# Kernel optimization log

Hardware: AMD Instinct MI355X
Metric: run time of the kernel (lower is better)

Reference implementation:

```python
import jax, jax.numpy as jnp
import numpy as np

NUM_CHUNKS = 8
HEAD_DIM = 128
PROJ = 1024       # projection_size (q)
KV_PROJ = 1024    # kv_projection_size
NEG_INF = -1e30


def _rotate_half(x):
    x1, x2 = jnp.split(x, 2, axis=-1)
    return jnp.concatenate((-x2, x1), axis=-1)


def _apply_rope(x, cos, sin):
    # x: [B, S, H, D]; cos/sin: [B, S, 1, rot_dim] with rot_dim == D here
    return x * cos + _rotate_half(x) * sin


def setup_inputs() -> dict:
    key = jax.random.key(0)
    k1, k2, k3 = jax.random.split(key, 3)
    S, B, H = 8192, 1, 1024
    layernorm_output = jax.random.normal(k1, (S, B, H), dtype=jnp.float32)
    # rotary tables, stored [S, 1, 1, rot_dim] (seq-first, like the torch module)
    inv_freq = 1.0 / (10000.0 ** (jnp.arange(0, HEAD_DIM, 2, dtype=jnp.float32) / HEAD_DIM))
    t = jnp.arange(S, dtype=jnp.float32)
    freqs = jnp.einsum('s,d->sd', t, inv_freq)
    emb = jnp.concatenate((freqs, freqs), axis=-1)  # [S, rot_dim]
    freqs_cos = jnp.cos(emb)[:, None, None, :]
    freqs_sin = jnp.sin(emb)[:, None, None, :]
    qkv_weight = jax.random.normal(k2, (PROJ + 2 * KV_PROJ, H), dtype=jnp.float32) * (H ** -0.5)
    qkv_bias = jax.random.normal(k3, (PROJ + 2 * KV_PROJ,), dtype=jnp.float32) * 0.02
    return {
        'layernorm_output': layernorm_output,
        'freqs_cos': freqs_cos,
        'freqs_sin': freqs_sin,
        'qkv_weight': qkv_weight,
        'qkv_bias': qkv_bias,
    }


def reference(layernorm_output, freqs_cos, freqs_sin, qkv_weight, qkv_bias):
    S, B, H = layernorm_output.shape
    cs = S // NUM_CHUNKS  # chunk size
    scale = HEAD_DIM ** -0.5
    # permute(1,0,2,3): [S,1,1,rot] -> [1,S,1,rot] matching [B, seq, head, dim]
    cos = jnp.transpose(freqs_cos, (1, 0, 2, 3))
    sin = jnp.transpose(freqs_sin, (1, 0, 2, 3))

    outs = []
    k_list, v_list = [], []
    for i in range(NUM_CHUNKS):
        st, ed = i * cs, (i + 1) * cs
        x = layernorm_output[st:ed]                      # [cs, B, H]
        qkv = jnp.einsum('sbh,oh->sbo', x, qkv_weight) + qkv_bias
        def to_bshd(t):
            return jnp.transpose(t.reshape(cs, B, -1, HEAD_DIM), (1, 0, 2, 3))
        q = to_bshd(qkv[..., :PROJ])                     # [B, cs, nH, D]
        k = to_bshd(qkv[..., PROJ:PROJ + KV_PROJ])
        v = to_bshd(qkv[..., PROJ + KV_PROJ:])
        cos_i, sin_i = cos[:, st:ed], sin[:, st:ed]
        q = _apply_rope(q, cos_i, sin_i)
        k = _apply_rope(k, cos_i, sin_i)
        k_list.append(k)
        v_list.append(v)

        K = jnp.concatenate(k_list, axis=1)              # [B, (i+1)*cs, nH, D]
        V = jnp.concatenate(v_list, axis=1)
        scores = jnp.einsum('bqhd,bkhd->bhqk', q, K) * scale
        # causal: query global idx st+r attends keys <= st+r; earlier chunks fully visible
        qidx = st + jnp.arange(cs)
        kidx = jnp.arange((i + 1) * cs)
        mask = kidx[None, :] <= qidx[:, None]            # [cs, (i+1)*cs]
        scores = jnp.where(mask[None, None], scores, NEG_INF)
        p = jax.nn.softmax(scores, axis=-1)
        outs.append(jnp.einsum('bhqk,bkhd->bqhd', p, V))
    return jnp.concatenate(outs, axis=1)                 # [B, S, nH, D]
```

## Files before the change

### kernel.cpp

```cpp
#include <hip/hip_runtime.h>
#include <hip/hip_bf16.h>

typedef float f32x4 __attribute__((ext_vector_type(4)));
typedef __bf16 bf16x8 __attribute__((ext_vector_type(8)));
typedef __bf16 bf16x4 __attribute__((ext_vector_type(4)));

#define S_LEN 8192
#define HIDDEN 1024
#define NH 8
#define HD 128

#define QSCALE (0.08838834764831845f * 1.4426950408889634f)
#define FIXMAX 24.0f

__device__ __forceinline__ void async16(const void* g, void* l) {
  __builtin_amdgcn_global_load_lds(
      (const __attribute__((address_space(1))) char*)g,
      (__attribute__((address_space(3))) char*)l, 16, 0, 0);
}

__global__ void cast_bf16_kernel(const float* __restrict__ in, __bf16* __restrict__ out) {
  int i = (blockIdx.x * blockDim.x + threadIdx.x) * 4;
  float4 v = *(const float4*)(in + i);
  bf16x4 o;
  o[0] = (__bf16)v.x; o[1] = (__bf16)v.y; o[2] = (__bf16)v.z; o[3] = (__bf16)v.w;
  *(bf16x4*)(out + i) = o;
}

__global__ __launch_bounds__(256) void gemm_qkv(
    const __bf16* __restrict__ A, const __bf16* __restrict__ W,
    const float* __restrict__ bias,
    __bf16* __restrict__ Qb, __bf16* __restrict__ Kb, __bf16* __restrict__ Vt)
{
  __shared__ __bf16 As[128 * 32];
  __shared__ __bf16 Bs[128 * 32];
  const int t = threadIdx.x;
  const int lane = t & 63;
  const int w = t >> 6;
  const int wy = w >> 1, wx = w & 1;
  const int quad = lane >> 4, l15 = lane & 15;
  const int m0 = blockIdx.y * 128;
  const int n0 = blockIdx.x * 128;
  f32x4 acc[4][4] = {};
  for (int kt = 0; kt < HIDDEN; kt += 32) {
#pragma unroll
    for (int j = 0; j < 2; ++j) {
      int idx = j * 256 + t;
      int row = idx >> 2, c8 = (idx & 3) * 8;
      async16(A + (size_t)(m0 + row) * HIDDEN + kt + c8, As + idx * 8);
      async16(W + (size_t)(n0 + row) * HIDDEN + kt + c8, Bs + idx * 8);
    }
    __syncthreads();
    bf16x8 af[4], bfr[4];
#pragma unroll
    for (int i = 0; i < 4; ++i)
      af[i] = *(const bf16x8*)(As + (wy * 64 + i * 16 + l15) * 32 + quad * 8);
#pragma unroll
    for (int i = 0; i < 4; ++i)
      bfr[i] = *(const bf16x8*)(Bs + (wx * 64 + i * 16 + l15) * 32 + quad * 8);
#pragma unroll
    for (int mt = 0; mt < 4; ++mt)
#pragma unroll
      for (int nt = 0; nt < 4; ++nt)
        acc[mt][nt] = __builtin_amdgcn_mfma_f32_16x16x32_bf16(af[mt], bfr[nt], acc[mt][nt], 0, 0, 0);
    __syncthreads();
  }
  float bv[4];
  int cols[4];
#pragma unroll
  for (int nt = 0; nt < 4; ++nt) {
    cols[nt] = n0 + wx * 64 + nt * 16 + l15;
    bv[nt] = bias[cols[nt]];
  }
#pragma unroll
  for (int mt = 0; mt < 4; ++mt) {
    int srow_base = m0 + wy * 64 + mt * 16 + quad * 4;
#pragma unroll
    for (int nt = 0; nt < 4; ++nt) {
      int c = cols[nt];
#pragma unroll
      for (int r = 0; r < 4; ++r) {
        int s = srow_base + r;
        __bf16 b = (__bf16)(acc[mt][nt][r] + bv[nt]);
        if (n0 < 1024) {
          int h = c >> 7, d = c & 127;
          Qb[(size_t)h * S_LEN * HD + (size_t)s * HD + d] = b;
        } else if (n0 < 2048) {
          int c2 = c - 1024; int h = c2 >> 7, d = c2 & 127;
          Kb[(size_t)h * S_LEN * HD + (size_t)s * HD + d] = b;
        } else {
          int c2 = c - 2048; int h = c2 >> 7, d = c2 & 127;
          Vt[(size_t)h * HD * S_LEN + (size_t)d * S_LEN + s] = b;
        }
      }
    }
  }
}

__global__ void rope_kernel(__bf16* __restrict__ Qb, __bf16* __restrict__ Kb,
                            const float* __restrict__ fcos, const float* __restrict__ fsin)
{
  int gid = blockIdx.x * blockDim.x + threadIdx.x;
  int d = gid & 63;
  int h = (gid >> 6) & 7;
  int s = gid >> 9;
  float c1 = fcos[s * 128 + d],      s1 = fsin[s * 128 + d];
  float c2 = fcos[s * 128 + d + 64], s2 = fsin[s * 128 + d + 64];
  size_t base = (size_t)h * S_LEN * HD + (size_t)s * HD + d;
  float q1 = (float)Qb[base], q2 = (float)Qb[base + 64];
  Qb[base]      = (__bf16)((q1 * c1 - q2 * s1) * QSCALE);
  Qb[base + 64] = (__bf16)((q2 * c2 + q1 * s2) * QSCALE);
  float k1 = (float)Kb[base], k2 = (float)Kb[base + 64];
  Kb[base]      = (__bf16)(k1 * c1 - k2 * s1);
  Kb[base + 64] = (__bf16)(k2 * c2 + k1 * s2);
}

__global__ __launch_bounds__(256, 2) void attn_kernel(
    const __bf16* __restrict__ Qb, const __bf16* __restrict__ Kb,
    const __bf16* __restrict__ Vt, float* __restrict__ out,
    __bf16* __restrict__ partO, float* __restrict__ partML)
{
  __shared__ __bf16 Ks[2][64 * 128];
  __shared__ __bf16 Vs[2][128 * 64];
  __shared__ __bf16 Ps[4 * 16 * 64];
  const int t = threadIdx.x;
  const int lane = t & 63, w = t >> 6;
  const int quad = lane >> 4, l15 = lane & 15;
  const int sw = l15 & 7;
  const int sw4 = (l15 & 3) << 2;

  const int id = blockIdx.x;
  const int k = id / 24, r = id % 24;
  int head, qi, piece, j0, j1;
  bool isPartial;
  if (r < 16) { qi = 63 - k; piece = r >> 3; head = r & 7;
                j0 = piece * (qi + 1); j1 = j0 + (qi + 1); isPartial = true; }
  else        { qi = 31 - k; piece = 0; head = r - 16;
                j0 = 0; j1 = 2 * qi + 2; isPartial = false; }
  const int qs = qi * 128;
  const int jmax_w = 2 * qi + (w >> 1);
  const __bf16* Qh = Qb + (size_t)head * S_LEN * HD;
  const __bf16* Kh = Kb + (size_t)head * S_LEN * HD;
  const __bf16* Vh = Vt + (size_t)head * HD * S_LEN;

  bf16x8 qf[2][4];
#pragma unroll
  for (int qg = 0; qg < 2; ++qg) {
    int qrow = qs + w * 32 + qg * 16 + l15;
#pragma unroll
    for (int dk = 0; dk < 4; ++dk)
      qf[qg][dk] = *(const bf16x8*)(Qh + (size_t)qrow * HD + dk * 32 + quad * 8);
  }

  f32x4 o[2][8] = {};
  float l_loc[2] = {0.f, 0.f};
  const f32x4 FM = {-FIXMAX, -FIXMAX, -FIXMAX, -FIXMAX};

  auto stageK = [&](int j, int sel) {
    const __bf16* Kp = Kh + (size_t)(j * 64) * HD;
    __bf16* Kd = &Ks[sel][0];
#pragma unroll
    for (int li = 0; li < 4; ++li) {
      int slot = li * 256 + t;
      int kr = slot >> 4, cp = slot & 15;
      async16(Kp + (size_t)kr * HD + (cp ^ (kr & 7)) * 8, Kd + slot * 8);
    }
  };
  auto stageV = [&](int j, int sel) {
    const __bf16* Vp = Vh + j * 64;
    __bf16* Vd = &Vs[sel][0];
#pragma unroll
    for (int li = 0; li < 4; ++li) {
      int slot = li * 256 + t;
      int d = slot >> 3, cp = slot & 7;
      async16(Vp + (size_t)d * S_LEN + (cp ^ (d & 7)) * 8, Vd + slot * 8);
    }
  };

  stageK(j0, 0);
  stageV(j0, 0);

  for (int j = j0; j < j1; ++j) {
    __syncthreads();
    const int cur = (j - j0) & 1;
    if (j + 1 < j1) {
      stageK(j + 1, cur ^ 1);
      stageV(j + 1, cur ^ 1);
    }
    if (j > jmax_w) continue;
    const __bf16* Ksb = &Ks[cur][0];
    const __bf16* Vsb = &Vs[cur][0];

    f32x4 sc[2][4];
#pragma unroll
    for (int mtk = 0; mtk < 4; ++mtk) {
      bf16x8 kf = *(const bf16x8*)(Ksb + (mtk * 16 + l15) * 128 + ((quad ^ sw) * 8));
      sc[0][mtk] = __builtin_amdgcn_mfma_f32_16x16x32_bf16(kf, qf[0][0], FM, 0, 0, 0);
      sc[1][mtk] = __builtin_amdgcn_mfma_f32_16x16x32_bf16(kf, qf[1][0], FM, 0, 0, 0);
    }
#pragma unroll
    for (int dk = 1; dk < 4; ++dk)
#pragma unroll
      for (int mtk = 0; mtk < 4; ++mtk) {
        bf16x8 kf = *(const bf16x8*)(Ksb + (mtk * 16 + l15) * 128 + (((dk * 4 + quad) ^ sw) * 8));
        sc[0][mtk] = __builtin_amdgcn_mfma_f32_16x16x32_bf16(kf, qf[0][dk], sc[0][mtk], 0, 0, 0);
        sc[1][mtk] = __builtin_amdgcn_mfma_f32_16x16x32_bf16(kf, qf[1][dk], sc[1][mtk], 0, 0, 0);
      }

    if (j >= 2 * qi && (w >> 1) == (j - 2 * qi)) {
      int wq = (w & 1) * 32;
#pragma unroll
      for (int qg = 0; qg < 2; ++qg)
#pragma unroll
        for (int mtk = 0; mtk < 4; ++mtk)
#pragma unroll
          for (int r2 = 0; r2 < 4; ++r2)
            if (mtk * 16 + quad * 4 + r2 - wq > qg * 16 + l15)
              sc[qg][mtk][r2] = -1e30f;
    }

    bf16x8 vf[2][8];
#pragma unroll
    for (int kb = 0; kb < 2; ++kb)
#pragma unroll
      for (int dt = 0; dt < 8; ++dt)
        vf[kb][dt] = *(const bf16x8*)(Vsb + (dt * 16 + l15) * 64 + (((kb * 4 + quad) ^ sw) * 8));

#pragma unroll
    for (int qg = 0; qg < 2; ++qg) {
#pragma unroll
      for (int mtk = 0; mtk < 4; ++mtk) {
        bf16x4 pk;
#pragma unroll
        for (int r2 = 0; r2 < 4; ++r2) {
          float p = __builtin_amdgcn_exp2f(sc[qg][mtk][r2]);
          l_loc[qg] += p;
          pk[r2] = (__bf16)p;
        }
        int slot = (mtk * 4 + quad) ^ sw4;
        *(bf16x4*)(Ps + w * 1024 + l15 * 64 + slot * 4) = pk;
      }
#pragma unroll
      for (int kb = 0; kb < 2; ++kb) {
        bf16x8 pf = *(const bf16x8*)(Ps + w * 1024 + l15 * 64 + (((kb * 8 + quad * 2) ^ sw4) * 4));
#pragma unroll
        for (int dt = 0; dt < 8; ++dt)
          o[qg][dt] = __builtin_amdgcn_mfma_f32_16x16x32_bf16(vf[kb][dt], pf, o[qg][dt], 0, 0, 0);
      }
    }
  }

  float inv[2], lfull[2];
#pragma unroll
  for (int qg = 0; qg < 2; ++qg) {
    float lv = l_loc[qg];
    lv += __shfl_xor(lv, 16);
    lv += __shfl_xor(lv, 32);
    lfull[qg] = lv;
    inv[qg] = 1.0f / lv;
  }
  if (!isPartial) {
#pragma unroll
    for (int qg = 0; qg < 2; ++qg) {
      int s = qs + w * 32 + qg * 16 + l15;
#pragma unroll
      for (int dt = 0; dt < 8; ++dt) {
        f32x4 v;
#pragma unroll
        for (int r2 = 0; r2 < 4; ++r2) v[r2] = o[qg][dt][r2] * inv[qg];
        *(f32x4*)(out + (size_t)s * 1024 + head * 128 + dt * 16 + quad * 4) = v;
      }
    }
  } else {
    int u = (qi - 32) * 16 + piece * 8 + head;
    __bf16* Op = partO + (size_t)u * 128 * 128;
    float* mlp = partML + u * 256;
#pragma unroll
    for (int qg = 0; qg < 2; ++qg) {
      int row = w * 32 + qg * 16 + l15;
#pragma unroll
      for (int dt = 0; dt < 8; ++dt) {
        bf16x4 pk;
#pragma unroll
        for (int r2 = 0; r2 < 4; ++r2) pk[r2] = (__bf16)(o[qg][dt][r2] * inv[qg]);
        *(bf16x4*)(Op + row * 128 + dt * 16 + quad * 4) = pk;
      }
    }
    if (quad == 0) {
#pragma unroll
      for (int qg = 0; qg < 2; ++qg)
        mlp[w * 32 + qg * 16 + l15] = lfull[qg];
    }
  }
}

__global__ __launch_bounds__(256) void merge_kernel(
    const __bf16* __restrict__ partO, const float* __restrict__ partML,
    float* __restrict__ out)
{
  int b = blockIdx.x;
  int qi = 32 + (b >> 3), head = b & 7;
  int u0 = (qi - 32) * 16 + head;
  int u1 = u0 + 8;
  int t = threadIdx.x;
  int q = t >> 1, dh = (t & 1) * 64;
  float l0 = partML[u0 * 256 + q];
  float l1 = partML[u1 * 256 + q];
  float inv = 1.0f / (l0 + l1);
  float w0 = l0 * inv, w1 = l1 * inv;
  const __bf16* O0 = partO + ((size_t)u0 * 128 + q) * 128 + dh;
  const __bf16* O1 = partO + ((size_t)u1 * 128 + q) * 128 + dh;
  float* op = out + (size_t)(qi * 128 + q) * 1024 + head * 128 + dh;
#pragma unroll
  for (int d = 0; d < 64; d += 8) {
    bf16x8 a = *(const bf16x8*)(O0 + d);
    bf16x8 c = *(const bf16x8*)(O1 + d);
    float4 r0, r1;
    r0.x = w0 * (float)a[0] + w1 * (float)c[0];
    r0.y = w0 * (float)a[1] + w1 * (float)c[1];
    r0.z = w0 * (float)a[2] + w1 * (float)c[2];
    r0.w = w0 * (float)a[3] + w1 * (float)c[3];
    r1.x = w0 * (float)a[4] + w1 * (float)c[4];
    r1.y = w0 * (float)a[5] + w1 * (float)c[5];
    r1.z = w0 * (float)a[6] + w1 * (float)c[6];
    r1.w = w0 * (float)a[7] + w1 * (float)c[7];
    *(float4*)(op + d) = r0;
    *(float4*)(op + d + 4) = r1;
  }
}

extern "C" void kernel_launch(void* const* d_in, const int* in_sizes, int n_in,
                              void* d_out, int out_size, void* d_ws, size_t ws_size,
                              hipStream_t stream)
{
  const float* x    = (const float*)d_in[0];
  const float* fcos = (const float*)d_in[1];
  const float* fsin = (const float*)d_in[2];
  const float* wq   = (const float*)d_in[3];
  const float* bias = (const float*)d_in[4];
  float* out = (float*)d_out;

  char* ws = (char*)d_ws;
  __bf16* xb = (__bf16*)ws;
  __bf16* wb = (__bf16*)(ws + 16777216);
  __bf16* Qb = (__bf16*)(ws + 23068672);
  __bf16* Kb = (__bf16*)(ws + 39845888);
  __bf16* Vt = (__bf16*)(ws + 56623104);

  __bf16* partO = xb;
  float* partML = (float*)wb;

  cast_bf16_kernel<<<8192, 256, 0, stream>>>(x, xb);
  cast_bf16_kernel<<<3072, 256, 0, stream>>>(wq, wb);
  dim3 gg(24, 64);
  gemm_qkv<<<gg, 256, 0, stream>>>(xb, wb, bias, Qb, Kb, Vt);
  rope_kernel<<<16384, 256, 0, stream>>>(Qb, Kb, fcos, fsin);
  attn_kernel<<<768, 256, 0, stream>>>(Qb, Kb, Vt, out, partO, partML);
  merge_kernel<<<256, 256, 0, stream>>>(partO, partML, out);
}
```

Measured before the change: 427.9 us.

## Use 256-row query tiles with 512-thread blocks and split every tile's KV range

Result: slower. 916.8 us (+114.2%).

```diff
diff --git a/kernel.cpp b/kernel.cpp
--- a/kernel.cpp
+++ b/kernel.cpp
@@ -115,14 +115,14 @@
   Kb[base + 64] = (__bf16)(k2 * c2 + k1 * s2);
 }
 
-__global__ __launch_bounds__(256, 2) void attn_kernel(
+__global__ __launch_bounds__(512, 4) void attn_kernel(
     const __bf16* __restrict__ Qb, const __bf16* __restrict__ Kb,
     const __bf16* __restrict__ Vt, float* __restrict__ out,
     __bf16* __restrict__ partO, float* __restrict__ partML)
 {
   __shared__ __bf16 Ks[2][64 * 128];
   __shared__ __bf16 Vs[2][128 * 64];
-  __shared__ __bf16 Ps[4 * 16 * 64];
+  __shared__ __bf16 Ps[8 * 16 * 64];
   const int t = threadIdx.x;
   const int lane = t & 63, w = t >> 6;
   const int quad = lane >> 4, l15 = lane & 15;
@@ -130,15 +130,15 @@
   const int sw4 = (l15 & 3) << 2;
 
   const int id = blockIdx.x;
-  const int k = id / 24, r = id % 24;
-  int head, qi, piece, j0, j1;
-  bool isPartial;
-  if (r < 16) { qi = 63 - k; piece = r >> 3; head = r & 7;
-                j0 = piece * (qi + 1); j1 = j0 + (qi + 1); isPartial = true; }
-  else        { qi = 31 - k; piece = 0; head = r - 16;
-                j0 = 0; j1 = 2 * qi + 2; isPartial = false; }
-  const int qs = qi * 128;
-  const int jmax_w = 2 * qi + (w >> 1);
+  int qs, r;
+  if (id < 256) { qs = 31 - (id >> 4); r = id & 15; }
+  else          { qs = (id - 256) >> 4; r = id & 15; }
+  const int piece = r >> 3, head = r & 7;
+  const int nt = 2 * qs + 2;
+  const int j0 = piece * nt, j1 = j0 + nt;
+  const int jmax_w = 4 * qs + (w >> 1);
+  const int qbase = qs * 256;
+
   const __bf16* Qh = Qb + (size_t)head * S_LEN * HD;
   const __bf16* Kh = Kb + (size_t)head * S_LEN * HD;
   const __bf16* Vh = Vt + (size_t)head * HD * S_LEN;
@@ -146,7 +146,7 @@
   bf16x8 qf[2][4];
 #pragma unroll
   for (int qg = 0; qg < 2; ++qg) {
-    int qrow = qs + w * 32 + qg * 16 + l15;
+    int qrow = qbase + w * 32 + qg * 16 + l15;
 #pragma unroll
     for (int dk = 0; dk < 4; ++dk)
       qf[qg][dk] = *(const bf16x8*)(Qh + (size_t)qrow * HD + dk * 32 + quad * 8);
@@ -160,8 +160,8 @@
     const __bf16* Kp = Kh + (size_t)(j * 64) * HD;
     __bf16* Kd = &Ks[sel][0];
 #pragma unroll
-    for (int li = 0; li < 4; ++li) {
-      int slot = li * 256 + t;
+    for (int li = 0; li < 2; ++li) {
+      int slot = li * 512 + t;
       int kr = slot >> 4, cp = slot & 15;
       async16(Kp + (size_t)kr * HD + (cp ^ (kr & 7)) * 8, Kd + slot * 8);
     }
@@ -170,8 +170,8 @@
     const __bf16* Vp = Vh + j * 64;
     __bf16* Vd = &Vs[sel][0];
 #pragma unroll
-    for (int li = 0; li < 4; ++li) {
-      int slot = li * 256 + t;
+    for (int li = 0; li < 2; ++li) {
+      int slot = li * 512 + t;
       int d = slot >> 3, cp = slot & 7;
       async16(Vp + (size_t)d * S_LEN + (cp ^ (d & 7)) * 8, Vd + slot * 8);
     }
@@ -207,7 +207,7 @@
         sc[1][mtk] = __builtin_amdgcn_mfma_f32_16x16x32_bf16(kf, qf[1][dk], sc[1][mtk], 0, 0, 0);
       }
 
-    if (j >= 2 * qi && (w >> 1) == (j - 2 * qi)) {
+    if (j == jmax_w) {
       int wq = (w & 1) * 32;
 #pragma unroll
       for (int qg = 0; qg < 2; ++qg)
@@ -257,12 +257,12 @@
     lv += __shfl_xor(lv, 16);
     lv += __shfl_xor(lv, 32);
     lfull[qg] = lv;
-    inv[qg] = 1.0f / lv;
-  }
-  if (!isPartial) {
+    inv[qg] = lv > 0.f ? 1.0f / lv : 0.f;
+  }
+  if (piece == 1) {
 #pragma unroll
     for (int qg = 0; qg < 2; ++qg) {
-      int s = qs + w * 32 + qg * 16 + l15;
+      int s = qbase + w * 32 + qg * 16 + l15;
 #pragma unroll
       for (int dt = 0; dt < 8; ++dt) {
         f32x4 v;
@@ -272,9 +272,7 @@
       }
     }
   } else {
-    int u = (qi - 32) * 16 + piece * 8 + head;
-    __bf16* Op = partO + (size_t)u * 128 * 128;
-    float* mlp = partML + u * 256;
+    __bf16* Op = partO + (size_t)(qs * 8 + head) * 256 * 128;
 #pragma unroll
     for (int qg = 0; qg < 2; ++qg) {
       int row = w * 32 + qg * 16 + l15;
@@ -286,6 +284,9 @@
         *(bf16x4*)(Op + row * 128 + dt * 16 + quad * 4) = pk;
       }
     }
+  }
+  {
+    float* mlp = partML + (size_t)(qs * 16 + piece * 8 + head) * 256;
     if (quad == 0) {
 #pragma unroll
       for (int qg = 0; qg < 2; ++qg)
@@ -299,33 +300,26 @@
     float* __restrict__ out)
 {
   int b = blockIdx.x;
-  int qi = 32 + (b >> 3), head = b & 7;
-  int u0 = (qi - 32) * 16 + head;
-  int u1 = u0 + 8;
+  int qs = b >> 3, head = b & 7;
   int t = threadIdx.x;
-  int q = t >> 1, dh = (t & 1) * 64;
-  float l0 = partML[u0 * 256 + q];
-  float l1 = partML[u1 * 256 + q];
-  float inv = 1.0f / (l0 + l1);
-  float w0 = l0 * inv, w1 = l1 * inv;
-  const __bf16* O0 = partO + ((size_t)u0 * 128 + q) * 128 + dh;
-  const __bf16* O1 = partO + ((size_t)u1 * 128 + q) * 128 + dh;
-  float* op = out + (size_t)(qi * 128 + q) * 1024 + head * 128 + dh;
-#pragma unroll
-  for (int d = 0; d < 64; d += 8) {
-    bf16x8 a = *(const bf16x8*)(O0 + d);
-    bf16x8 c = *(const bf16x8*)(O1 + d);
-    float4 r0, r1;
-    r0.x = w0 * (float)a[0] + w1 * (float)c[0];
-    r0.y = w0 * (float)a[1] + w1 * (float)c[1];
-    r0.z = w0 * (float)a[2] + w1 * (float)c[2];
-    r0.w = w0 * (float)a[3] + w1 * (float)c[3];
-    r1.x = w0 * (float)a[4] + w1 * (float)c[4];
-    r1.y = w0 * (float)a[5] + w1 * (float)c[5];
-    r1.z = w0 * (float)a[6] + w1 * (float)c[6];
-    r1.w = w0 * (float)a[7] + w1 * (float)c[7];
-    *(float4*)(op + d) = r0;
-    *(float4*)(op + d + 4) = r1;
+  int dq = (t & 31) * 4;
+  const float* ml0 = partML + (size_t)(qs * 16 + head) * 256;
+  const float* ml1 = partML + (size_t)(qs * 16 + 8 + head) * 256;
+  const __bf16* O0 = partO + (size_t)(qs * 8 + head) * 256 * 128;
+#pragma unroll 4
+  for (int row = t >> 5; row < 256; row += 8) {
+    float l0 = ml0[row];
+    float l1 = ml1[row];
+    float inv = 1.0f / (l0 + l1);
+    float w0 = l0 * inv, w1 = l1 * inv;
+    bf16x4 a = *(const bf16x4*)(O0 + row * 128 + dq);
+    float* op = out + (size_t)(qs * 256 + row) * 1024 + head * 128 + dq;
+    float4 c = *(const float4*)op;
+    c.x = w0 * (float)a[0] + w1 * c.x;
+    c.y = w0 * (float)a[1] + w1 * c.y;
+    c.z = w0 * (float)a[2] + w1 * c.z;
+    c.w = w0 * (float)a[3] + w1 * c.w;
+    *(float4*)op = c;
   }
 }
 
@@ -355,6 +349,6 @@
   dim3 gg(24, 64);
   gemm_qkv<<<gg, 256, 0, stream>>>(xb, wb, bias, Qb, Kb, Vt);
   rope_kernel<<<16384, 256, 0, stream>>>(Qb, Kb, fcos, fsin);
-  attn_kernel<<<768, 256, 0, stream>>>(Qb, Kb, Vt, out, partO, partML);
+  attn_kernel<<<512, 512, 0, stream>>>(Qb, Kb, Vt, out, partO, partML);
   merge_kernel<<<256, 256, 0, stream>>>(partO, partML, out);
 }
```

## Halve attention KV tile to 32 keys and raise occupancy to three blocks

Applied to the files above, without the earlier changes.

Result: faster. 384.2 us (-10.2%).

```diff
diff --git a/kernel.cpp b/kernel.cpp
--- a/kernel.cpp
+++ b/kernel.cpp
@@ -115,30 +115,30 @@
   Kb[base + 64] = (__bf16)(k2 * c2 + k1 * s2);
 }
 
-__global__ __launch_bounds__(256, 2) void attn_kernel(
+__global__ __launch_bounds__(256, 3) void attn_kernel(
     const __bf16* __restrict__ Qb, const __bf16* __restrict__ Kb,
     const __bf16* __restrict__ Vt, float* __restrict__ out,
     __bf16* __restrict__ partO, float* __restrict__ partML)
 {
-  __shared__ __bf16 Ks[2][64 * 128];
-  __shared__ __bf16 Vs[2][128 * 64];
-  __shared__ __bf16 Ps[4 * 16 * 64];
+  __shared__ __bf16 Ks[2][32 * 128];
+  __shared__ __bf16 Vs[2][64 * 64];
+  __shared__ __bf16 Ps[4 * 1024];
   const int t = threadIdx.x;
   const int lane = t & 63, w = t >> 6;
   const int quad = lane >> 4, l15 = lane & 15;
   const int sw = l15 & 7;
-  const int sw4 = (l15 & 3) << 2;
+  const int sw6 = l15 & 6;
 
   const int id = blockIdx.x;
   const int k = id / 24, r = id % 24;
   int head, qi, piece, j0, j1;
   bool isPartial;
   if (r < 16) { qi = 63 - k; piece = r >> 3; head = r & 7;
-                j0 = piece * (qi + 1); j1 = j0 + (qi + 1); isPartial = true; }
+                j0 = piece * (2 * qi + 2); j1 = j0 + (2 * qi + 2); isPartial = true; }
   else        { qi = 31 - k; piece = 0; head = r - 16;
-                j0 = 0; j1 = 2 * qi + 2; isPartial = false; }
+                j0 = 0; j1 = 4 * qi + 4; isPartial = false; }
   const int qs = qi * 128;
-  const int jmax_w = 2 * qi + (w >> 1);
+  const int jmax_w = 4 * qi + w;
   const __bf16* Qh = Qb + (size_t)head * S_LEN * HD;
   const __bf16* Kh = Kb + (size_t)head * S_LEN * HD;
   const __bf16* Vh = Vt + (size_t)head * HD * S_LEN;
@@ -157,23 +157,25 @@
   const f32x4 FM = {-FIXMAX, -FIXMAX, -FIXMAX, -FIXMAX};
 
   auto stageK = [&](int j, int sel) {
-    const __bf16* Kp = Kh + (size_t)(j * 64) * HD;
+    const __bf16* Kp = Kh + (size_t)(j * 32) * HD;
     __bf16* Kd = &Ks[sel][0];
 #pragma unroll
-    for (int li = 0; li < 4; ++li) {
+    for (int li = 0; li < 2; ++li) {
       int slot = li * 256 + t;
       int kr = slot >> 4, cp = slot & 15;
       async16(Kp + (size_t)kr * HD + (cp ^ (kr & 7)) * 8, Kd + slot * 8);
     }
   };
   auto stageV = [&](int j, int sel) {
-    const __bf16* Vp = Vh + j * 64;
+    const __bf16* Vp = Vh + j * 32;
     __bf16* Vd = &Vs[sel][0];
 #pragma unroll
-    for (int li = 0; li < 4; ++li) {
-      int slot = li * 256 + t;
-      int d = slot >> 3, cp = slot & 7;
-      async16(Vp + (size_t)d * S_LEN + (cp ^ (d & 7)) * 8, Vd + slot * 8);
+    for (int li = 0; li < 2; ++li) {
+      int c = li * 256 + t;
+      int rr = c >> 3, sl = c & 7;
+      int slu = sl ^ (rr & 7);
+      int d = 2 * rr + (slu >> 2);
+      async16(Vp + (size_t)d * S_LEN + (slu & 3) * 8, Vd + c * 8);
     }
   };
 
@@ -191,9 +193,9 @@
     const __bf16* Ksb = &Ks[cur][0];
     const __bf16* Vsb = &Vs[cur][0];
 
-    f32x4 sc[2][4];
-#pragma unroll
-    for (int mtk = 0; mtk < 4; ++mtk) {
+    f32x4 sc[2][2];
+#pragma unroll
+    for (int mtk = 0; mtk < 2; ++mtk) {
       bf16x8 kf = *(const bf16x8*)(Ksb + (mtk * 16 + l15) * 128 + ((quad ^ sw) * 8));
       sc[0][mtk] = __builtin_amdgcn_mfma_f32_16x16x32_bf16(kf, qf[0][0], FM, 0, 0, 0);
       sc[1][mtk] = __builtin_amdgcn_mfma_f32_16x16x32_bf16(kf, qf[1][0], FM, 0, 0, 0);
@@ -201,35 +203,27 @@
 #pragma unroll
     for (int dk = 1; dk < 4; ++dk)
 #pragma unroll
-      for (int mtk = 0; mtk < 4; ++mtk) {
+      for (int mtk = 0; mtk < 2; ++mtk) {
         bf16x8 kf = *(const bf16x8*)(Ksb + (mtk * 16 + l15) * 128 + (((dk * 4 + quad) ^ sw) * 8));
         sc[0][mtk] = __builtin_amdgcn_mfma_f32_16x16x32_bf16(kf, qf[0][dk], sc[0][mtk], 0, 0, 0);
         sc[1][mtk] = __builtin_amdgcn_mfma_f32_16x16x32_bf16(kf, qf[1][dk], sc[1][mtk], 0, 0, 0);
       }
 
-    if (j >= 2 * qi && (w >> 1) == (j - 2 * qi)) {
-      int wq = (w & 1) * 32;
+    if (j == jmax_w) {
 #pragma unroll
       for (int qg = 0; qg < 2; ++qg)
 #pragma unroll
-        for (int mtk = 0; mtk < 4; ++mtk)
+        for (int mtk = 0; mtk < 2; ++mtk)
 #pragma unroll
           for (int r2 = 0; r2 < 4; ++r2)
-            if (mtk * 16 + quad * 4 + r2 - wq > qg * 16 + l15)
+            if (mtk * 16 + quad * 4 + r2 > qg * 16 + l15)
               sc[qg][mtk][r2] = -1e30f;
     }
 
-    bf16x8 vf[2][8];
-#pragma unroll
-    for (int kb = 0; kb < 2; ++kb)
-#pragma unroll
-      for (int dt = 0; dt < 8; ++dt)
-        vf[kb][dt] = *(const bf16x8*)(Vsb + (dt * 16 + l15) * 64 + (((kb * 4 + quad) ^ sw) * 8));
-
-#pragma unroll
-    for (int qg = 0; qg < 2; ++qg) {
-#pragma unroll
-      for (int mtk = 0; mtk < 4; ++mtk) {
+#pragma unroll
+    for (int qg = 0; qg < 2; ++qg)
+#pragma unroll
+      for (int mtk = 0; mtk < 2; ++mtk) {
         bf16x4 pk;
 #pragma unroll
         for (int r2 = 0; r2 < 4; ++r2) {
@@ -237,16 +231,23 @@
           l_loc[qg] += p;
           pk[r2] = (__bf16)p;
         }
-        int slot = (mtk * 4 + quad) ^ sw4;
-        *(bf16x4*)(Ps + w * 1024 + l15 * 64 + slot * 4) = pk;
-      }
-#pragma unroll
-      for (int kb = 0; kb < 2; ++kb) {
-        bf16x8 pf = *(const bf16x8*)(Ps + w * 1024 + l15 * 64 + (((kb * 8 + quad * 2) ^ sw4) * 4));
-#pragma unroll
-        for (int dt = 0; dt < 8; ++dt)
-          o[qg][dt] = __builtin_amdgcn_mfma_f32_16x16x32_bf16(vf[kb][dt], pf, o[qg][dt], 0, 0, 0);
-      }
+        int slot = (mtk * 4 + quad) ^ sw6;
+        *(bf16x4*)(Ps + w * 1024 + qg * 512 + l15 * 32 + slot * 4) = pk;
+      }
+
+    bf16x8 pf[2];
+#pragma unroll
+    for (int qg = 0; qg < 2; ++qg)
+      pf[qg] = *(const bf16x8*)(Ps + w * 1024 + qg * 512 + l15 * 32 + (((quad * 2) ^ sw6) * 4));
+
+#pragma unroll
+    for (int dt = 0; dt < 8; ++dt) {
+      int d = dt * 16 + l15;
+      int rr = d >> 1;
+      int slu = ((d & 1) << 2) | quad;
+      bf16x8 vf = *(const bf16x8*)(Vsb + rr * 64 + ((slu ^ (rr & 7)) * 8));
+      o[0][dt] = __builtin_amdgcn_mfma_f32_16x16x32_bf16(vf, pf[0], o[0][dt], 0, 0, 0);
+      o[1][dt] = __builtin_amdgcn_mfma_f32_16x16x32_bf16(vf, pf[1], o[1][dt], 0, 0, 0);
     }
   }
 
```
